# Kernel tuning notes

Measured on AMD Instinct MI355X. Metric: run time of the kernel, lower is better.

The kernel has to match this reference:

```python
import jax, jax.numpy as jnp
import numpy as np

H, W, WS, HEADS = 112, 112, 7, 8
DIM, HID = 512, 2048


def _layernorm(x, g, b, eps=1e-5):
    mu = jnp.mean(x, axis=-1, keepdims=True)
    var = jnp.var(x, axis=-1, keepdims=True)
    return (x - mu) * jax.lax.rsqrt(var + eps) * g + b


def _cpe(x, w, b):
    # depthwise 3x3 conv positional encoding with residual; x: [B, L, C]
    B, L, C = x.shape
    img = x.reshape(B, H, W, C)
    feat = jax.lax.conv_general_dilated(
        img, w, window_strides=(1, 1), padding='SAME',
        dimension_numbers=('NHWC', 'HWIO', 'NHWC'), feature_group_count=C) + b
    return x + feat.reshape(B, L, C)


def _window_partition(x):
    # [B, H, W, C] -> [B*nW, ws*ws, C]
    B, _, _, C = x.shape
    x = x.reshape(B, H // WS, WS, W // WS, WS, C)
    x = jnp.transpose(x, (0, 1, 3, 2, 4, 5))
    return x.reshape(-1, WS * WS, C)


def _window_reverse(xw, B):
    # [B*nW, ws*ws, C] -> [B, H*W, C]
    C = xw.shape[-1]
    x = xw.reshape(B, H // WS, W // WS, WS, WS, C)
    x = jnp.transpose(x, (0, 1, 3, 2, 4, 5))
    return x.reshape(B, H * W, C)


def _attention(x, qkv_w, qkv_b, proj_w, proj_b):
    # x: [nW, N, C]; standard MHA within each window
    nW, N, C = x.shape
    d = C // HEADS
    qkv = x @ qkv_w + qkv_b                      # [nW, N, 3C]
    qkv = qkv.reshape(nW, N, 3, HEADS, d)
    q, k, v = qkv[:, :, 0], qkv[:, :, 1], qkv[:, :, 2]  # [nW, N, h, d]
    scale = d ** -0.5
    attn = jnp.einsum('wqhd,wkhd->whqk', q * scale, k)
    attn = jax.nn.softmax(attn, axis=-1)
    out = jnp.einsum('whqk,wkhd->wqhd', attn, v).reshape(nW, N, C)
    return out @ proj_w + proj_b


def setup_inputs() -> dict:
    key = jax.random.key(0)
    ks = jax.random.split(key, 16)
    s = 0.02
    return {
        'x': jax.random.normal(ks[0], (4, H * W, DIM), jnp.float32),
        'cpe0_w': jax.random.normal(ks[1], (3, 3, 1, DIM), jnp.float32) * s,
        'cpe0_b': jnp.zeros((DIM,), jnp.float32),
        'cpe1_w': jax.random.normal(ks[2], (3, 3, 1, DIM), jnp.float32) * s,
        'cpe1_b': jnp.zeros((DIM,), jnp.float32),
        'ln1_g': jnp.ones((DIM,), jnp.float32),
        'ln1_b': jnp.zeros((DIM,), jnp.float32),
        'ln2_g': jnp.ones((DIM,), jnp.float32),
        'ln2_b': jnp.zeros((DIM,), jnp.float32),
        'qkv_w': jax.random.normal(ks[3], (DIM, 3 * DIM), jnp.float32) * s,
        'qkv_b': jnp.zeros((3 * DIM,), jnp.float32),
        'attn_proj_w': jax.random.normal(ks[4], (DIM, DIM), jnp.float32) * s,
        'attn_proj_b': jnp.zeros((DIM,), jnp.float32),
        'fc1_w': jax.random.normal(ks[5], (DIM, HID), jnp.float32) * s,
        'fc1_b': jnp.zeros((HID,), jnp.float32),
        'fc2_w': jax.random.normal(ks[6], (HID, DIM), jnp.float32) * s,
        'fc2_b': jnp.zeros((DIM,), jnp.float32),
    }


def reference(x, cpe0_w, cpe0_b, cpe1_w, cpe1_b, ln1_g, ln1_b, ln2_g, ln2_b,
              qkv_w, qkv_b, attn_proj_w, attn_proj_b, fc1_w, fc1_b, fc2_w, fc2_b):
    B, L, C = x.shape
    shortcut = _cpe(x, cpe0_w, cpe0_b)                 # CPE #1 (with residual)
    h = _layernorm(shortcut, ln1_g, ln1_b)
    h = _window_partition(h.reshape(B, H, W, C))       # [B*nW, 49, C]
    h = _attention(h, qkv_w, qkv_b, attn_proj_w, attn_proj_b)
    h = _window_reverse(h, B)                          # [B, L, C]
    h = shortcut + h
    h = _cpe(h, cpe1_w, cpe1_b)                        # CPE #2 (with residual)
    m = _layernorm(h, ln2_g, ln2_b)
    m = jax.nn.gelu(m @ fc1_w + fc1_b) @ fc2_w + fc2_b
    return h + m
```

## Files before the change

kernel.cpp:

```cpp
#include <hip/hip_runtime.h>
#include <stdint.h>

#define HH 112
#define WW 112
#define CC 512
#define BB 4
#define LLEN (HH*WW)
#define NTOK (BB*LLEN)
#define NHEADS 8
#define HD 64
#define HIDDEN 2048

typedef __bf16 bf16x8 __attribute__((ext_vector_type(8)));
typedef float f32x4 __attribute__((ext_vector_type(4)));
typedef long i64;

__device__ __forceinline__ unsigned short f2bf(float x) {
  uint32_t u = __float_as_uint(x);
  u += 0x7fffu + ((u >> 16) & 1u);
  return (unsigned short)(u >> 16);
}
__device__ __forceinline__ float bf2f(unsigned short h) {
  return __uint_as_float((uint32_t)h << 16);
}
__device__ __forceinline__ int cvt4_fp8(float a, float b, float c, float d) {
  int r = 0;
  r = __builtin_amdgcn_cvt_pk_fp8_f32(a, b, r, false);
  r = __builtin_amdgcn_cvt_pk_fp8_f32(c, d, r, true);
  return r;
}

__device__ __forceinline__ void gload16(const void* gptr, void* lptr) {
  __builtin_amdgcn_global_load_lds(
      (const __attribute__((address_space(1))) void*)gptr,
      (__attribute__((address_space(3))) void*)lptr,
      16, 0, 0);
}

#define WAITV3() asm volatile("s_waitcnt vmcnt(3)" ::: "memory")
#define WAITV0() asm volatile("s_waitcnt vmcnt(0)" ::: "memory")
#define BAR() __builtin_amdgcn_s_barrier()
#define WAITL() do { asm volatile("s_waitcnt lgkmcnt(0)" ::: "memory"); \
                     __builtin_amdgcn_sched_barrier(0); } while (0)

__global__ __launch_bounds__(256) void wtranspose8_kernel(
    const float* __restrict__ w, unsigned char* __restrict__ wt, int K, int N) {
  int idx = blockIdx.x * 256 + threadIdx.x;
  if (idx >= K * N) return;
  int n = idx / K, k = idx - n * K;
  float v = w[(size_t)k * N + n] * 32.f;
  int r = __builtin_amdgcn_cvt_pk_fp8_f32(v, v, 0, false);
  wt[idx] = (unsigned char)r;
}

template <int INBF, int OUTBF>
__global__ __launch_bounds__(256) void cpe_kernel(
    const void* __restrict__ xin, const float* __restrict__ w,
    const float* __restrict__ bias, void* __restrict__ outp) {
  int tid = blockIdx.x * 256 + threadIdx.x;
  int c = (tid & 127) << 2;
  int pix = tid >> 7;
  int xx = pix % WW; int t2 = pix / WW; int yy = t2 % HH; int bb = t2 / HH;
  float4 bv = *(const float4*)(&bias[c]);
  float ax = bv.x, ay = bv.y, az = bv.z, aw = bv.w;
  auto ld = [&](size_t eo) -> float4 {
    float4 v;
    if (INBF) {
      uint2 u = *(const uint2*)(&((const unsigned short*)xin)[eo]);
      v.x = bf2f((unsigned short)(u.x & 0xffff));
      v.y = bf2f((unsigned short)(u.x >> 16));
      v.z = bf2f((unsigned short)(u.y & 0xffff));
      v.w = bf2f((unsigned short)(u.y >> 16));
    } else {
      v = *(const float4*)(&((const float*)xin)[eo]);
    }
    return v;
  };
  #pragma unroll
  for (int ky = 0; ky < 3; ky++) {
    int y = yy + ky - 1;
    if ((unsigned)y >= (unsigned)HH) continue;
    #pragma unroll
    for (int kx = 0; kx < 3; kx++) {
      int x2 = xx + kx - 1;
      if ((unsigned)x2 >= (unsigned)WW) continue;
      float4 v = ld((((size_t)bb * HH + y) * WW + x2) * CC + c);
      const float4 wv = *(const float4*)(&w[(ky * 3 + kx) * CC + c]);
      ax = fmaf(v.x, wv.x, ax); ay = fmaf(v.y, wv.y, ay);
      az = fmaf(v.z, wv.z, az); aw = fmaf(v.w, wv.w, aw);
    }
  }
  size_t o = (size_t)pix * CC + c;
  float4 xv = ld(o);
  float rx = xv.x + ax, ry = xv.y + ay, rz = xv.z + az, rw = xv.w + aw;
  if (OUTBF) {
    uint2 pk;
    pk.x = (uint32_t)f2bf(rx) | ((uint32_t)f2bf(ry) << 16);
    pk.y = (uint32_t)f2bf(rz) | ((uint32_t)f2bf(rw) << 16);
    *(uint2*)(&((unsigned short*)outp)[o]) = pk;
  } else {
    float4 r; r.x = rx; r.y = ry; r.z = rz; r.w = rw;
    *(float4*)(&((float*)outp)[o]) = r;
  }
}

template <int INBF>
__global__ __launch_bounds__(256) void ln_kernel(
    const void* __restrict__ in, const float* __restrict__ g,
    const float* __restrict__ b, unsigned char* __restrict__ out8) {
  int token = (blockIdx.x * 256 + threadIdx.x) >> 6;
  int lane = threadIdx.x & 63;
  float v[8];
  if (INBF) {
    uint4 u = *(const uint4*)(&((const unsigned short*)in)[(size_t)token * CC + lane * 8]);
    v[0] = bf2f((unsigned short)(u.x & 0xffff)); v[1] = bf2f((unsigned short)(u.x >> 16));
    v[2] = bf2f((unsigned short)(u.y & 0xffff)); v[3] = bf2f((unsigned short)(u.y >> 16));
    v[4] = bf2f((unsigned short)(u.z & 0xffff)); v[5] = bf2f((unsigned short)(u.z >> 16));
    v[6] = bf2f((unsigned short)(u.w & 0xffff)); v[7] = bf2f((unsigned short)(u.w >> 16));
  } else {
    const float* row = (const float*)in + (size_t)token * CC;
    float4 a = *(const float4*)(row + lane * 8);
    float4 c4 = *(const float4*)(row + lane * 8 + 4);
    v[0] = a.x; v[1] = a.y; v[2] = a.z; v[3] = a.w;
    v[4] = c4.x; v[5] = c4.y; v[6] = c4.z; v[7] = c4.w;
  }
  float s = 0.f, ss = 0.f;
  #pragma unroll
  for (int i = 0; i < 8; i++) { s += v[i]; ss += v[i] * v[i]; }
  #pragma unroll
  for (int o = 32; o; o >>= 1) { s += __shfl_xor(s, o, 64); ss += __shfl_xor(ss, o, 64); }
  float mu = s * (1.f / CC);
  float var = ss * (1.f / CC) - mu * mu;
  float rs = rsqrtf(var + 1e-5f);
  float4 g0 = *(const float4*)(&g[lane * 8]);
  float4 g1 = *(const float4*)(&g[lane * 8 + 4]);
  float4 b0 = *(const float4*)(&b[lane * 8]);
  float4 b1 = *(const float4*)(&b[lane * 8 + 4]);
  float o8[8];
  o8[0] = (v[0] - mu) * rs * g0.x + b0.x;
  o8[1] = (v[1] - mu) * rs * g0.y + b0.y;
  o8[2] = (v[2] - mu) * rs * g0.z + b0.z;
  o8[3] = (v[3] - mu) * rs * g0.w + b0.w;
  o8[4] = (v[4] - mu) * rs * g1.x + b1.x;
  o8[5] = (v[5] - mu) * rs * g1.y + b1.y;
  o8[6] = (v[6] - mu) * rs * g1.z + b1.z;
  o8[7] = (v[7] - mu) * rs * g1.w + b1.w;
  uint2 pk;
  pk.x = (uint32_t)cvt4_fp8(o8[0], o8[1], o8[2], o8[3]);
  pk.y = (uint32_t)cvt4_fp8(o8[4], o8[5], o8[6], o8[7]);
  *(uint2*)(&out8[(size_t)token * CC + lane * 8]) = pk;
}

#define BM 256
#define BN 128
#define BK8 64

template <int MODE>
__global__ __launch_bounds__(512) void gemm8_kernel(
    const unsigned char* __restrict__ A, const unsigned char* __restrict__ BT,
    const float* __restrict__ bias, const float* __restrict__ res,
    const unsigned short* __restrict__ resB,
    float* __restrict__ outF, unsigned char* __restrict__ outB8,
    unsigned short* __restrict__ outB16, int M, int N, int K) {
  __shared__ unsigned char ldsb[49152];
  int nwg = gridDim.x * gridDim.y;
  int flat = blockIdx.y * gridDim.x + blockIdx.x;
  int swz = (flat & 7) * (nwg >> 3) + (flat >> 3);
  int bx = swz % gridDim.x, by = swz / gridDim.x;
  const int bm = by * BM, bn = bx * BN;
  const int t = threadIdx.x;
  const int wid = t >> 6, lane = t & 63;
  const int wr = wid >> 1, wc = wid & 1;
  const int lr = lane & 15, g = lane >> 4;
  const int swr = (lr >> 1) & 3;
  const int rb0 = (((g >> 1)      ) ^ swr) * 16 + (g & 1) * 8;
  const int rb1 = (((g >> 1) + 2) ^ swr) * 16 + (g & 1) * 8;
  const int srow = t >> 2;
  const int scol = (((t & 3) ^ ((t >> 3) & 3)) & 3) * 16;
  const size_t arow0 = (size_t)(bm + srow) * K + scol;
  const size_t arow1 = (size_t)(bm + 128 + srow) * K + scol;
  const size_t brow  = (size_t)(bn + srow) * K + scol;
  const int ldso = wid * 1024;

#define STG8(b, kt) do { \
    gload16(&A[arow0 + (kt)], ldsb + (b) * 16384 + ldso); \
    gload16(&A[arow1 + (kt)], ldsb + (b) * 16384 + 8192 + ldso); \
    gload16(&BT[brow + (kt)], ldsb + 32768 + (b) * 8192 + ldso); } while (0)

  f32x4 acc[4][4] = {};
  const int nt = K / BK8;

  STG8(0, 0);
  STG8(1, BK8);

  for (int tile = 0; tile < nt - 1; ++tile) {
    WAITV3(); BAR();
    const unsigned char* as = ldsb + (tile & 1) * 16384;
    const unsigned char* bs = ldsb + 32768 + (tile & 1) * 8192;
    i64 af0[4], af1[4], bf0[4], bf1[4];
    #pragma unroll
    for (int i = 0; i < 4; i++) {
      const unsigned char* p = &as[(wr * 64 + i * 16 + lr) * BK8];
      af0[i] = *(const i64*)(p + rb0);
      af1[i] = *(const i64*)(p + rb1);
    }
    #pragma unroll
    for (int j = 0; j < 4; j++) {
      const unsigned char* p = &bs[(wc * 64 + j * 16 + lr) * BK8];
      bf0[j] = *(const i64*)(p + rb0);
      bf1[j] = *(const i64*)(p + rb1);
    }
    WAITL();
    BAR();
    if (tile + 2 < nt) STG8(tile & 1, (tile + 2) * BK8);
    __builtin_amdgcn_s_setprio(1);
    #pragma unroll
    for (int i = 0; i < 4; i++)
      #pragma unroll
      for (int j = 0; j < 4; j++) {
        acc[i][j] = __builtin_amdgcn_mfma_f32_16x16x32_fp8_fp8(af0[i], bf0[j], acc[i][j], 0, 0, 0);
        acc[i][j] = __builtin_amdgcn_mfma_f32_16x16x32_fp8_fp8(af1[i], bf1[j], acc[i][j], 0, 0, 0);
      }
    __builtin_amdgcn_s_setprio(0);
  }
  {
    WAITV0(); BAR();
    const unsigned char* as = ldsb + ((nt - 1) & 1) * 16384;
    const unsigned char* bs = ldsb + 32768 + ((nt - 1) & 1) * 8192;
    i64 af0[4], af1[4], bf0[4], bf1[4];
    #pragma unroll
    for (int i = 0; i < 4; i++) {
      const unsigned char* p = &as[(wr * 64 + i * 16 + lr) * BK8];
      af0[i] = *(const i64*)(p + rb0);
      af1[i] = *(const i64*)(p + rb1);
    }
    #pragma unroll
    for (int j = 0; j < 4; j++) {
      const unsigned char* p = &bs[(wc * 64 + j * 16 + lr) * BK8];
      bf0[j] = *(const i64*)(p + rb0);
      bf1[j] = *(const i64*)(p + rb1);
    }
    WAITL();
    #pragma unroll
    for (int i = 0; i < 4; i++)
      #pragma unroll
      for (int j = 0; j < 4; j++) {
        acc[i][j] = __builtin_amdgcn_mfma_f32_16x16x32_fp8_fp8(af0[i], bf0[j], acc[i][j], 0, 0, 0);
        acc[i][j] = __builtin_amdgcn_mfma_f32_16x16x32_fp8_fp8(af1[i], bf1[j], acc[i][j], 0, 0, 0);
      }
  }
#undef STG8

  {
    const float SC = 0.03125f;
    float* eps = (float*)ldsb;
    const int erow = t >> 3;
    const int ecol0 = (t & 7) * 16;
    const int wrow = wr * 16 + (lane >> 4) * 4;
    const int wcol = wc * 64 + lr;
    const int gr_base = bm + (erow >> 4) * 64 + (erow & 15);
    const int gc0 = bn + ecol0;
    float bv[16];
    #pragma unroll
    for (int c4 = 0; c4 < 4; c4++)
      *(float4*)&bv[c4 * 4] = *(const float4*)&bias[gc0 + c4 * 4];
    #pragma unroll
    for (int i = 0; i < 4; i++) {
      __syncthreads();
      #pragma unroll
      for (int j = 0; j < 4; j++)
        #pragma unroll
        for (int r = 0; r < 4; r++)
          eps[(wrow + r) * 132 + wcol + j * 16] = acc[i][j][r];
      __syncthreads();
      float vv[16];
      #pragma unroll
      for (int c4 = 0; c4 < 4; c4++)
        *(float4*)&vv[c4 * 4] = *(const float4*)&eps[erow * 132 + ecol0 + c4 * 4];
      const size_t off = (size_t)(gr_base + i * 16) * N + gc0;
      if (MODE == 1) {
        #pragma unroll
        for (int c4 = 0; c4 < 4; c4++) {
          float4 rv = *(const float4*)&res[off + c4 * 4];
          float4 ov;
          ov.x = vv[c4*4+0] * SC + bv[c4*4+0] + rv.x;
          ov.y = vv[c4*4+1] * SC + bv[c4*4+1] + rv.y;
          ov.z = vv[c4*4+2] * SC + bv[c4*4+2] + rv.z;
          ov.w = vv[c4*4+3] * SC + bv[c4*4+3] + rv.w;
          *(float4*)&outF[off + c4 * 4] = ov;
        }
      } else if (MODE == 0) {
        uint4 pk;
        pk.x = (uint32_t)cvt4_fp8(vv[0]*SC+bv[0],  vv[1]*SC+bv[1],  vv[2]*SC+bv[2],  vv[3]*SC+bv[3]);
        pk.y = (uint32_t)cvt4_fp8(vv[4]*SC+bv[4],  vv[5]*SC+bv[5],  vv[6]*SC+bv[6],  vv[7]*SC+bv[7]);
        pk.z = (uint32_t)cvt4_fp8(vv[8]*SC+bv[8],  vv[9]*SC+bv[9],  vv[10]*SC+bv[10], vv[11]*SC+bv[11]);
        pk.w = (uint32_t)cvt4_fp8(vv[12]*SC+bv[12], vv[13]*SC+bv[13], vv[14]*SC+bv[14], vv[15]*SC+bv[15]);
        *(uint4*)&outB8[off] = pk;
      } else if (MODE == 3) {
        uint4 r0 = *(const uint4*)&resB[off];
        uint4 r1 = *(const uint4*)&resB[off + 8];
        unsigned short ob[16];
        const uint32_t* rp = (const uint32_t*)&r0;
        #pragma unroll
        for (int c = 0; c < 8; c++) {
          uint32_t u = rp[c >> 1];
          float rv = bf2f((unsigned short)((c & 1) ? (u >> 16) : (u & 0xffff)));
          ob[c] = f2bf(vv[c] * SC + bv[c] + rv);
        }
        const uint32_t* rp1 = (const uint32_t*)&r1;
        #pragma unroll
        for (int c = 0; c < 8; c++) {
          uint32_t u = rp1[c >> 1];
          float rv = bf2f((unsigned short)((c & 1) ? (u >> 16) : (u & 0xffff)));
          ob[8 + c] = f2bf(vv[8 + c] * SC + bv[8 + c] + rv);
        }
        *(uint4*)&outB16[off]     = *(uint4*)&ob[0];
        *(uint4*)&outB16[off + 8] = *(uint4*)&ob[8];
      } else {
        float gv[16];
        #pragma unroll
        for (int c = 0; c < 16; c++) {
          float v = vv[c] * SC + bv[c];
          float a2 = v * v;
          float w = v * fmaf(a2, -0.1029436f, -2.3024849f);
          float sg = __builtin_amdgcn_rcpf(1.f + __builtin_amdgcn_exp2f(w));
          gv[c] = v * sg;
        }
        uint4 pk;
        pk.x = (uint32_t)cvt4_fp8(gv[0],  gv[1],  gv[2],  gv[3]);
        pk.y = (uint32_t)cvt4_fp8(gv[4],  gv[5],  gv[6],  gv[7]);
        pk.z = (uint32_t)cvt4_fp8(gv[8],  gv[9],  gv[10], gv[11]);
        pk.w = (uint32_t)cvt4_fp8(gv[12], gv[13], gv[14], gv[15]);
        *(uint4*)&outB8[off] = pk;
      }
    }
  }
}

#define WNS8 72

__global__ __launch_bounds__(64) void attn_mfma8_kernel(
    const unsigned char* __restrict__ qkv, unsigned char* __restrict__ out) {
  __shared__ unsigned char VT[64 * WNS8];
  __shared__ unsigned char Ps[64 * WNS8];
  const int task = blockIdx.x;
  const int win = task >> 3, h = task & 7;
  const int b = win >> 8, wy = (win >> 4) & 15, wx = win & 15;
  const int lane = threadIdx.x;
  const int lr = lane & 15, g = lane >> 4;

  auto tokof = [&](int r) {
    int rr = r > 48 ? 48 : r;
    int y = rr / 7, x2 = rr - y * 7;
    return (size_t)(b * LLEN + (wy * 7 + y) * WW + wx * 7 + x2);
  };

  {
    size_t vbase = tokof(lane) * 1536 + 1024 + h * 64;
    bool valid = lane <= 48;
    #pragma unroll
    for (int c = 0; c < 4; c++) {
      uint4 v = *(const uint4*)(&qkv[vbase + c * 16]);
      const unsigned char* pv = (const unsigned char*)&v;
      #pragma unroll
      for (int e = 0; e < 16; e++)
        VT[(c * 16 + e) * WNS8 + lane] = valid ? pv[e] : (unsigned char)0;
    }
  }

  size_t tok[4];
  #pragma unroll
  for (int i2 = 0; i2 < 4; i2++) tok[i2] = tokof(i2 * 16 + lr);
  i64 Qf[4][2], Kf[4][2];
  #pragma unroll
  for (int i2 = 0; i2 < 4; i2++) {
    size_t base = tok[i2] * 1536 + h * 64 + g * 8;
    #pragma unroll
    for (int ks = 0; ks < 2; ks++) {
      Qf[i2][ks] = *(const i64*)(&qkv[base + ks * 32]);
      Kf[i2][ks] = *(const i64*)(&qkv[base + 512 + ks * 32]);
    }
  }

  f32x4 acc[4][4] = {};
  #pragma unroll
  for (int ks = 0; ks < 2; ks++)
    #pragma unroll
    for (int i2 = 0; i2 < 4; i2++)
      #pragma unroll
      for (int j = 0; j < 4; j++)
        acc[i2][j] = __builtin_amdgcn_mfma_f32_16x16x32_fp8_fp8(Kf[i2][ks], Qf[j][ks], acc[i2][j], 0, 0, 0);

  #pragma unroll
  for (int j = 0; j < 4; j++) {
    float mx = -1e30f;
    #pragma unroll
    for (int i2 = 0; i2 < 4; i2++)
      #pragma unroll
      for (int r = 0; r < 4; r++) {
        int k = 16 * i2 + 4 * g + r;
        mx = fmaxf(mx, (k <= 48) ? acc[i2][j][r] : -1e30f);
      }
    mx = fmaxf(mx, __shfl_xor(mx, 16, 64));
    mx = fmaxf(mx, __shfl_xor(mx, 32, 64));
    float p[4][4];
    float sum = 0.f;
    #pragma unroll
    for (int i2 = 0; i2 < 4; i2++)
      #pragma unroll
      for (int r = 0; r < 4; r++) {
        int k = 16 * i2 + 4 * g + r;
        float e = (k <= 48) ? __expf(0.125f * (acc[i2][j][r] - mx)) : 0.f;
        p[i2][r] = e; sum += e;
      }
    sum += __shfl_xor(sum, 16, 64);
    sum += __shfl_xor(sum, 32, 64);
    float inv = 1.f / sum;
    int q = 16 * j + lr;
    #pragma unroll
    for (int i2 = 0; i2 < 4; i2++) {
      uint32_t w = (uint32_t)cvt4_fp8(p[i2][0] * inv, p[i2][1] * inv,
                                      p[i2][2] * inv, p[i2][3] * inv);
      *(uint32_t*)(&Ps[q * WNS8 + 16 * i2 + 4 * g]) = w;
    }
  }

  __syncthreads();

  f32x4 o[4][4] = {};
  #pragma unroll
  for (int ks = 0; ks < 2; ks++) {
    i64 Pf[4], Vf[4];
    #pragma unroll
    for (int i2 = 0; i2 < 4; i2++)
      Pf[i2] = *(const i64*)(&Ps[(16 * i2 + lr) * WNS8 + ks * 32 + g * 8]);
    #pragma unroll
    for (int j = 0; j < 4; j++)
      Vf[j] = *(const i64*)(&VT[(16 * j + lr) * WNS8 + ks * 32 + g * 8]);
    #pragma unroll
    for (int i2 = 0; i2 < 4; i2++)
      #pragma unroll
      for (int j = 0; j < 4; j++)
        o[i2][j] = __builtin_amdgcn_mfma_f32_16x16x32_fp8_fp8(Pf[i2], Vf[j], o[i2][j], 0, 0, 0);
  }

  #pragma unroll
  for (int i2 = 0; i2 < 4; i2++)
    #pragma unroll
    for (int r = 0; r < 4; r++) {
      int q = 16 * i2 + 4 * g + r;
      if (q <= 48) {
        size_t obase = tokof(q) * 512 + h * 64 + lr;
        #pragma unroll
        for (int j = 0; j < 4; j++) {
          float v = o[i2][j][r];
          int rr = __builtin_amdgcn_cvt_pk_fp8_f32(v, v, 0, false);
          out[obase + 16 * j] = (unsigned char)rr;
        }
      }
    }
}

extern "C" void kernel_launch(void* const* d_in, const int* in_sizes, int n_in,
                              void* d_out, int out_size, void* d_ws, size_t ws_size,
                              hipStream_t stream) {
  const float* x      = (const float*)d_in[0];
  const float* cpe0_w = (const float*)d_in[1];
  const float* cpe0_b = (const float*)d_in[2];
  const float* cpe1_w = (const float*)d_in[3];
  const float* cpe1_b = (const float*)d_in[4];
  const float* ln1_g  = (const float*)d_in[5];
  const float* ln1_b  = (const float*)d_in[6];
  const float* ln2_g  = (const float*)d_in[7];
  const float* ln2_b  = (const float*)d_in[8];
  const float* qkv_w  = (const float*)d_in[9];
  const float* qkv_b  = (const float*)d_in[10];
  const float* proj_w = (const float*)d_in[11];
  const float* proj_b = (const float*)d_in[12];
  const float* fc1_w  = (const float*)d_in[13];
  const float* fc1_b  = (const float*)d_in[14];
  const float* fc2_w  = (const float*)d_in[15];
  const float* fc2_b  = (const float*)d_in[16];
  float* out = (float*)d_out;
  char* ws = (char*)d_ws;

  unsigned char*  qkvwT8 = (unsigned char*)(ws + 0);
  unsigned char*  projwT8 = (unsigned char*)(ws + 1048576);
  unsigned char*  fc1wT8 = (unsigned char*)(ws + 2097152);
  unsigned char*  fc2wT8 = (unsigned char*)(ws + 4194304);
  unsigned short* shortcB = (unsigned short*)(ws + 6291456);
  unsigned char*  lnb8   = (unsigned char*)(ws + 109051904);
  unsigned char*  qkvb8  = (unsigned char*)(ws + 160432128);
  unsigned char*  attnb8 = (unsigned char*)(ws + 314572800);
  unsigned char*  gelub8 = (unsigned char*)(ws + 160432128);
  float* h2 = out;

  wtranspose8_kernel<<<(512 * 1536 + 255) / 256, 256, 0, stream>>>(qkv_w, qkvwT8, 512, 1536);
  wtranspose8_kernel<<<(512 * 512 + 255) / 256, 256, 0, stream>>>(proj_w, projwT8, 512, 512);
  wtranspose8_kernel<<<(512 * 2048 + 255) / 256, 256, 0, stream>>>(fc1_w, fc1wT8, 512, 2048);
  wtranspose8_kernel<<<(2048 * 512 + 255) / 256, 256, 0, stream>>>(fc2_w, fc2wT8, 2048, 512);

  const int pixblocks = (BB * HH * WW * 128) / 256;
  cpe_kernel<0, 1><<<pixblocks, 256, 0, stream>>>(x, cpe0_w, cpe0_b, shortcB);
  ln_kernel<1><<<NTOK / 4, 256, 0, stream>>>(shortcB, ln1_g, ln1_b, lnb8);
  gemm8_kernel<0><<<dim3(12, 196), 512, 0, stream>>>(lnb8, qkvwT8, qkv_b, nullptr,
      nullptr, nullptr, qkvb8, nullptr, NTOK, 1536, 512);
  attn_mfma8_kernel<<<8192, 64, 0, stream>>>(qkvb8, attnb8);
  gemm8_kernel<3><<<dim3(4, 196), 512, 0, stream>>>(attnb8, projwT8, proj_b, nullptr,
      shortcB, nullptr, nullptr, shortcB, NTOK, 512, 512);
  cpe_kernel<1, 0><<<pixblocks, 256, 0, stream>>>(shortcB, cpe1_w, cpe1_b, h2);
  ln_kernel<0><<<NTOK / 4, 256, 0, stream>>>(h2, ln2_g, ln2_b, lnb8);
  gemm8_kernel<2><<<dim3(16, 196), 512, 0, stream>>>(lnb8, fc1wT8, fc1_b, nullptr,
      nullptr, nullptr, gelub8, nullptr, NTOK, 2048, 512);
  gemm8_kernel<1><<<dim3(4, 196), 512, 0, stream>>>(gelub8, fc2wT8, fc2_b, h2,
      nullptr, out, nullptr, nullptr, NTOK, 512, 2048);
}
```

Measured before the change: 584.6 us.

## Add FP8 GEMM kernel using scaled 16x16x128 MFMA for QKV and MLP

```diff
diff --git a/kernel.cpp b/kernel.cpp
--- a/kernel.cpp
+++ b/kernel.cpp
@@ -13,6 +13,7 @@
 
 typedef __bf16 bf16x8 __attribute__((ext_vector_type(8)));
 typedef float f32x4 __attribute__((ext_vector_type(4)));
+typedef int i32x8 __attribute__((ext_vector_type(8)));
 typedef long i64;
 
 __device__ __forceinline__ unsigned short f2bf(float x) {
@@ -38,6 +39,7 @@
 }
 
 #define WAITV3() asm volatile("s_waitcnt vmcnt(3)" ::: "memory")
+#define WAITV8() asm volatile("s_waitcnt vmcnt(8)" ::: "memory")
 #define WAITV0() asm volatile("s_waitcnt vmcnt(0)" ::: "memory")
 #define BAR() __builtin_amdgcn_s_barrier()
 #define WAITL() do { asm volatile("s_waitcnt lgkmcnt(0)" ::: "memory"); \
@@ -158,9 +160,7 @@
 template <int MODE>
 __global__ __launch_bounds__(512) void gemm8_kernel(
     const unsigned char* __restrict__ A, const unsigned char* __restrict__ BT,
-    const float* __restrict__ bias, const float* __restrict__ res,
-    const unsigned short* __restrict__ resB,
-    float* __restrict__ outF, unsigned char* __restrict__ outB8,
+    const float* __restrict__ bias, const unsigned short* __restrict__ resB,
     unsigned short* __restrict__ outB16, int M, int N, int K) {
   __shared__ unsigned char ldsb[49152];
   int nwg = gridDim.x * gridDim.y;
@@ -278,60 +278,166 @@
       for (int c4 = 0; c4 < 4; c4++)
         *(float4*)&vv[c4 * 4] = *(const float4*)&eps[erow * 132 + ecol0 + c4 * 4];
       const size_t off = (size_t)(gr_base + i * 16) * N + gc0;
-      if (MODE == 1) {
+      uint4 r0 = *(const uint4*)&resB[off];
+      uint4 r1 = *(const uint4*)&resB[off + 8];
+      unsigned short ob[16];
+      const uint32_t* rp = (const uint32_t*)&r0;
+      #pragma unroll
+      for (int c = 0; c < 8; c++) {
+        uint32_t u = rp[c >> 1];
+        float rv = bf2f((unsigned short)((c & 1) ? (u >> 16) : (u & 0xffff)));
+        ob[c] = f2bf(vv[c] * SC + bv[c] + rv);
+      }
+      const uint32_t* rp1 = (const uint32_t*)&r1;
+      #pragma unroll
+      for (int c = 0; c < 8; c++) {
+        uint32_t u = rp1[c >> 1];
+        float rv = bf2f((unsigned short)((c & 1) ? (u >> 16) : (u & 0xffff)));
+        ob[8 + c] = f2bf(vv[8 + c] * SC + bv[8 + c] + rv);
+      }
+      *(uint4*)&outB16[off]     = *(uint4*)&ob[0];
+      *(uint4*)&outB16[off + 8] = *(uint4*)&ob[8];
+    }
+  }
+}
+
+__device__ __forceinline__ i32x8 ld_frag128(const unsigned char* base, int row, int g, int lrm7) {
+  const uint4 lo = *(const uint4*)(base + row * 128 + (((2 * g)     ^ lrm7) * 16));
+  const uint4 hi = *(const uint4*)(base + row * 128 + (((2 * g + 1) ^ lrm7) * 16));
+  i32x8 r;
+  r[0] = lo.x; r[1] = lo.y; r[2] = lo.z; r[3] = lo.w;
+  r[4] = hi.x; r[5] = hi.y; r[6] = hi.z; r[7] = hi.w;
+  return r;
+}
+
+template <int MODE>
+__global__ __launch_bounds__(256) void gemm8mx_kernel(
+    const unsigned char* __restrict__ A, const unsigned char* __restrict__ BT,
+    const float* __restrict__ bias, const float* __restrict__ res,
+    float* __restrict__ outF, unsigned char* __restrict__ outB8,
+    int M, int N, int K) {
+  __shared__ unsigned char ldsb[65536];
+  const int SCALE1 = 0x7F7F7F7F;
+  int nwg = gridDim.x * gridDim.y;
+  int flat = blockIdx.y * gridDim.x + blockIdx.x;
+  int swz = (flat & 7) * (nwg >> 3) + (flat >> 3);
+  int bx = swz % gridDim.x, by = swz / gridDim.x;
+  const int bm = by * 128, bn = bx * 128;
+  const int t = threadIdx.x;
+  const int wid = t >> 6, lane = t & 63;
+  const int wr = wid >> 1, wc = wid & 1;
+  const int lr = lane & 15, g = lane >> 4, lrm7 = lane & 7;
+  const int wq0 = wid * 4096;
+  const int scol = (((lane & 7) ^ ((lane >> 3) & 7)) & 7) * 16;
+  const size_t aB0 = (size_t)(bm + wid * 32 + ((t >> 3) & 7)) * K + scol;
+  const size_t bB0 = (size_t)(bn + wid * 32 + ((t >> 3) & 7)) * K + scol;
+
+#define STGMX(p, kt) do { \
+    _Pragma("unroll") for (int q_ = 0; q_ < 4; q_++) { \
+      gload16(&A[aB0 + (size_t)q_ * 8 * K + (kt)],  ldsb + (p) * 16384 + wq0 + q_ * 1024); \
+      gload16(&BT[bB0 + (size_t)q_ * 8 * K + (kt)], ldsb + 32768 + (p) * 16384 + wq0 + q_ * 1024); \
+    } } while (0)
+
+  f32x4 acc[4][4] = {};
+  const int npt = K / 128;
+
+  STGMX(0, 0);
+  STGMX(1, 128);
+
+  for (int pt = 0; pt < npt - 1; ++pt) {
+    WAITV8(); BAR();
+    const unsigned char* as = ldsb + (pt & 1) * 16384;
+    const unsigned char* bs = ldsb + 32768 + (pt & 1) * 16384;
+    i32x8 af[4], bf[4];
+    #pragma unroll
+    for (int i = 0; i < 4; i++)
+      af[i] = ld_frag128(as, wr * 64 + i * 16 + lr, g, lrm7);
+    #pragma unroll
+    for (int j = 0; j < 4; j++)
+      bf[j] = ld_frag128(bs, wc * 64 + j * 16 + lr, g, lrm7);
+    WAITL();
+    BAR();
+    if (pt + 2 < npt) STGMX(pt & 1, (pt + 2) * 128);
+    __builtin_amdgcn_s_setprio(1);
+    #pragma unroll
+    for (int i = 0; i < 4; i++)
+      #pragma unroll
+      for (int j = 0; j < 4; j++)
+        acc[i][j] = __builtin_amdgcn_mfma_scale_f32_16x16x128_f8f6f4(
+            af[i], bf[j], acc[i][j], 0, 0, 0, SCALE1, 0, SCALE1);
+    __builtin_amdgcn_s_setprio(0);
+  }
+  {
+    WAITV0(); BAR();
+    const unsigned char* as = ldsb + ((npt - 1) & 1) * 16384;
+    const unsigned char* bs = ldsb + 32768 + ((npt - 1) & 1) * 16384;
+    i32x8 af[4], bf[4];
+    #pragma unroll
+    for (int i = 0; i < 4; i++)
+      af[i] = ld_frag128(as, wr * 64 + i * 16 + lr, g, lrm7);
+    #pragma unroll
+    for (int j = 0; j < 4; j++)
+      bf[j] = ld_frag128(bs, wc * 64 + j * 16 + lr, g, lrm7);
+    WAITL();
+    #pragma unroll
+    for (int i = 0; i < 4; i++)
+      #pragma unroll
+      for (int j = 0; j < 4; j++)
+        acc[i][j] = __builtin_amdgcn_mfma_scale_f32_16x16x128_f8f6f4(
+            af[i], bf[j], acc[i][j], 0, 0, 0, SCALE1, 0, SCALE1);
+  }
+#undef STGMX
+
+  {
+    const float SC = 0.03125f;
+    float* eps = (float*)ldsb;
+    const int erow = t >> 2;
+    const int cb = (t & 3) * 4;
+    float4 bv4[8];
+    #pragma unroll
+    for (int c = 0; c < 8; c++)
+      bv4[c] = *(const float4*)&bias[bn + cb + c * 16];
+    #pragma unroll
+    for (int p = 0; p < 2; p++) {
+      __syncthreads();
+      if (wr == p) {
         #pragma unroll
-        for (int c4 = 0; c4 < 4; c4++) {
-          float4 rv = *(const float4*)&res[off + c4 * 4];
+        for (int i = 0; i < 4; i++)
+          #pragma unroll
+          for (int j = 0; j < 4; j++)
+            #pragma unroll
+            for (int r = 0; r < 4; r++)
+              eps[(i * 16 + g * 4 + r) * 132 + wc * 64 + j * 16 + lr] = acc[i][j][r];
+      }
+      __syncthreads();
+      const size_t rowoff = (size_t)(bm + p * 64 + erow) * N + bn + cb;
+      #pragma unroll
+      for (int c = 0; c < 8; c++) {
+        float4 vv = *(const float4*)&eps[erow * 132 + cb + c * 16];
+        float v0 = vv.x * SC + bv4[c].x;
+        float v1 = vv.y * SC + bv4[c].y;
+        float v2 = vv.z * SC + bv4[c].z;
+        float v3 = vv.w * SC + bv4[c].w;
+        if (MODE == 1) {
+          float4 rv = *(const float4*)&res[rowoff + c * 16];
           float4 ov;
-          ov.x = vv[c4*4+0] * SC + bv[c4*4+0] + rv.x;
-          ov.y = vv[c4*4+1] * SC + bv[c4*4+1] + rv.y;
-          ov.z = vv[c4*4+2] * SC + bv[c4*4+2] + rv.z;
-          ov.w = vv[c4*4+3] * SC + bv[c4*4+3] + rv.w;
-          *(float4*)&outF[off + c4 * 4] = ov;
+          ov.x = v0 + rv.x; ov.y = v1 + rv.y; ov.z = v2 + rv.z; ov.w = v3 + rv.w;
+          *(float4*)&outF[rowoff + c * 16] = ov;
+        } else if (MODE == 0) {
+          *(uint32_t*)&outB8[rowoff + c * 16] = (uint32_t)cvt4_fp8(v0, v1, v2, v3);
+        } else {
+          float gv[4];
+          float vin[4] = {v0, v1, v2, v3};
+          #pragma unroll
+          for (int e = 0; e < 4; e++) {
+            float v = vin[e];
+            float a2 = v * v;
+            float w = v * fmaf(a2, -0.1029436f, -2.3024849f);
+            float sg = __builtin_amdgcn_rcpf(1.f + __builtin_amdgcn_exp2f(w));
+            gv[e] = v * sg;
+          }
+          *(uint32_t*)&outB8[rowoff + c * 16] = (uint32_t)cvt4_fp8(gv[0], gv[1], gv[2], gv[3]);
         }
-      } else if (MODE == 0) {
-        uint4 pk;
-        pk.x = (uint32_t)cvt4_fp8(vv[0]*SC+bv[0],  vv[1]*SC+bv[1],  vv[2]*SC+bv[2],  vv[3]*SC+bv[3]);
-        pk.y = (uint32_t)cvt4_fp8(vv[4]*SC+bv[4],  vv[5]*SC+bv[5],  vv[6]*SC+bv[6],  vv[7]*SC+bv[7]);
-        pk.z = (uint32_t)cvt4_fp8(vv[8]*SC+bv[8],  vv[9]*SC+bv[9],  vv[10]*SC+bv[10], vv[11]*SC+bv[11]);
-        pk.w = (uint32_t)cvt4_fp8(vv[12]*SC+bv[12], vv[13]*SC+bv[13], vv[14]*SC+bv[14], vv[15]*SC+bv[15]);
-        *(uint4*)&outB8[off] = pk;
-      } else if (MODE == 3) {
-        uint4 r0 = *(const uint4*)&resB[off];
-        uint4 r1 = *(const uint4*)&resB[off + 8];
-        unsigned short ob[16];
-        const uint32_t* rp = (const uint32_t*)&r0;
-        #pragma unroll
-        for (int c = 0; c < 8; c++) {
-          uint32_t u = rp[c >> 1];
-          float rv = bf2f((unsigned short)((c & 1) ? (u >> 16) : (u & 0xffff)));
-          ob[c] = f2bf(vv[c] * SC + bv[c] + rv);
-        }
-        const uint32_t* rp1 = (const uint32_t*)&r1;
-        #pragma unroll
-        for (int c = 0; c < 8; c++) {
-          uint32_t u = rp1[c >> 1];
-          float rv = bf2f((unsigned short)((c & 1) ? (u >> 16) : (u & 0xffff)));
-          ob[8 + c] = f2bf(vv[8 + c] * SC + bv[8 + c] + rv);
-        }
-        *(uint4*)&outB16[off]     = *(uint4*)&ob[0];
-        *(uint4*)&outB16[off + 8] = *(uint4*)&ob[8];
-      } else {
-        float gv[16];
-        #pragma unroll
-        for (int c = 0; c < 16; c++) {
-          float v = vv[c] * SC + bv[c];
-          float a2 = v * v;
-          float w = v * fmaf(a2, -0.1029436f, -2.3024849f);
-          float sg = __builtin_amdgcn_rcpf(1.f + __builtin_amdgcn_exp2f(w));
-          gv[c] = v * sg;
-        }
-        uint4 pk;
-        pk.x = (uint32_t)cvt4_fp8(gv[0],  gv[1],  gv[2],  gv[3]);
-        pk.y = (uint32_t)cvt4_fp8(gv[4],  gv[5],  gv[6],  gv[7]);
-        pk.z = (uint32_t)cvt4_fp8(gv[8],  gv[9],  gv[10], gv[11]);
-        pk.w = (uint32_t)cvt4_fp8(gv[12], gv[13], gv[14], gv[15]);
-        *(uint4*)&outB8[off] = pk;
       }
     }
   }
@@ -503,15 +609,15 @@
   const int pixblocks = (BB * HH * WW * 128) / 256;
   cpe_kernel<0, 1><<<pixblocks, 256, 0, stream>>>(x, cpe0_w, cpe0_b, shortcB);
   ln_kernel<1><<<NTOK / 4, 256, 0, stream>>>(shortcB, ln1_g, ln1_b, lnb8);
-  gemm8_kernel<0><<<dim3(12, 196), 512, 0, stream>>>(lnb8, qkvwT8, qkv_b, nullptr,
-      nullptr, nullptr, qkvb8, nullptr, NTOK, 1536, 512);
+  gemm8mx_kernel<0><<<dim3(12, 392), 256, 0, stream>>>(lnb8, qkvwT8, qkv_b, nullptr,
+      nullptr, qkvb8, NTOK, 1536, 512);
   attn_mfma8_kernel<<<8192, 64, 0, stream>>>(qkvb8, attnb8);
-  gemm8_kernel<3><<<dim3(4, 196), 512, 0, stream>>>(attnb8, projwT8, proj_b, nullptr,
-      shortcB, nullptr, nullptr, shortcB, NTOK, 512, 512);
+  gemm8_kernel<3><<<dim3(4, 196), 512, 0, stream>>>(attnb8, projwT8, proj_b,
+      shortcB, shortcB, NTOK, 512, 512);
   cpe_kernel<1, 0><<<pixblocks, 256, 0, stream>>>(shortcB, cpe1_w, cpe1_b, h2);
   ln_kernel<0><<<NTOK / 4, 256, 0, stream>>>(h2, ln2_g, ln2_b, lnb8);
-  gemm8_kernel<2><<<dim3(16, 196), 512, 0, stream>>>(lnb8, fc1wT8, fc1_b, nullptr,
-      nullptr, nullptr, gelub8, nullptr, NTOK, 2048, 512);
-  gemm8_kernel<1><<<dim3(4, 196), 512, 0, stream>>>(gelub8, fc2wT8, fc2_b, h2,
-      nullptr, out, nullptr, nullptr, NTOK, 512, 2048);
-}
+  gemm8mx_kernel<2><<<dim3(16, 392), 256, 0, stream>>>(lnb8, fc1wT8, fc1_b, nullptr,
+      nullptr, gelub8, NTOK, 2048, 512);
+  gemm8mx_kernel<1><<<dim3(4, 392), 256, 0, stream>>>(gelub8, fc2wT8, fc2_b, h2,
+      out, nullptr, NTOK, 512, 2048);
+}
```

Result: faster. 558.7 us (-4.4%).
